# Kernel optimization log

Hardware: AMD Instinct MI355X
Metric: run time of the kernel (lower is better)

## Reference

```python
import jax, jax.numpy as jnp
import numpy as np

B = 262144
IN_DIM, HID, EXP, LAT, N_BLOCKS, N_CODES = 54, 256, 512, 32, 4, 512
EPS = 1e-5


def _layernorm(x, g, b):
    mu = jnp.mean(x, axis=-1, keepdims=True)
    var = jnp.mean(jnp.square(x - mu), axis=-1, keepdims=True)
    return (x - mu) * jax.lax.rsqrt(var + EPS) * g + b


def _blocks(h, ln_g, ln_b, w1, b1, w2, b2):
    # stacked params over n_blocks; small fixed loop over layers
    for i in range(N_BLOCKS):
        y = _layernorm(h, ln_g[i], ln_b[i])
        y = jax.nn.gelu(y @ w1[i] + b1[i], approximate=False)  # torch GELU = erf form
        h = h + (y @ w2[i] + b2[i])
    return h


def setup_inputs() -> dict:
    key = jax.random.key(0)
    ks = jax.random.split(key, 32)
    s = 0.02
    d = {
        "x": jax.random.normal(ks[0], (B, IN_DIM), jnp.float32),
        "enc_proj_w": jax.random.normal(ks[1], (IN_DIM, HID)) * s,
        "enc_proj_b": jnp.zeros((HID,)),
        "enc_ln_g": jnp.ones((N_BLOCKS, HID)),
        "enc_ln_b": jnp.zeros((N_BLOCKS, HID)),
        "enc_w1": jax.random.normal(ks[2], (N_BLOCKS, HID, EXP)) * s,
        "enc_b1": jnp.zeros((N_BLOCKS, EXP)),
        "enc_w2": jax.random.normal(ks[3], (N_BLOCKS, EXP, HID)) * s,
        "enc_b2": jnp.zeros((N_BLOCKS, HID)),
        "enc_norm_g": jnp.ones((HID,)),
        "enc_norm_b": jnp.zeros((HID,)),
        "enc_lat_w": jax.random.normal(ks[4], (HID, LAT)) * s,
        "enc_lat_b": jnp.zeros((LAT,)),
        "codebook": jax.random.normal(ks[5], (N_CODES, LAT)),
        "dec_lat_w": jax.random.normal(ks[6], (LAT, HID)) * s,
        "dec_lat_b": jnp.zeros((HID,)),
        "dec_ln_g": jnp.ones((N_BLOCKS, HID)),
        "dec_ln_b": jnp.zeros((N_BLOCKS, HID)),
        "dec_w1": jax.random.normal(ks[7], (N_BLOCKS, HID, EXP)) * s,
        "dec_b1": jnp.zeros((N_BLOCKS, EXP)),
        "dec_w2": jax.random.normal(ks[8], (N_BLOCKS, EXP, HID)) * s,
        "dec_b2": jnp.zeros((N_BLOCKS, HID)),
        "dec_norm_g": jnp.ones((HID,)),
        "dec_norm_b": jnp.zeros((HID,)),
        "dec_proj_w": jax.random.normal(ks[9], (HID, IN_DIM)) * s,
        "dec_proj_b": jnp.zeros((IN_DIM,)),
    }
    return {k: v.astype(jnp.float32) for k, v in d.items()}


def reference(x, enc_proj_w, enc_proj_b, enc_ln_g, enc_ln_b, enc_w1, enc_b1,
              enc_w2, enc_b2, enc_norm_g, enc_norm_b, enc_lat_w, enc_lat_b,
              codebook, dec_lat_w, dec_lat_b, dec_ln_g, dec_ln_b, dec_w1,
              dec_b1, dec_w2, dec_b2, dec_norm_g, dec_norm_b, dec_proj_w,
              dec_proj_b):
    # encode
    h = x @ enc_proj_w + enc_proj_b
    h = _blocks(h, enc_ln_g, enc_ln_b, enc_w1, enc_b1, enc_w2, enc_b2)
    h = _layernorm(h, enc_norm_g, enc_norm_b)
    z = h @ enc_lat_w + enc_lat_b  # (B, LAT)

    # VQ: nearest code by squared distance (same argmin as cdist)
    d2 = (jnp.sum(z * z, -1, keepdims=True)
          - 2.0 * (z @ codebook.T)
          + jnp.sum(codebook * codebook, -1))  # (B, N_CODES)
    indices = jnp.argmin(d2, axis=-1)
    z_q = codebook[indices]
    commit_loss = jnp.mean(jnp.square(z - jax.lax.stop_gradient(z_q)))
    z_q_st = z + jax.lax.stop_gradient(z_q - z)  # straight-through

    # decode
    h = z_q_st @ dec_lat_w + dec_lat_b
    h = _blocks(h, dec_ln_g, dec_ln_b, dec_w1, dec_b1, dec_w2, dec_b2)
    h = _layernorm(h, dec_norm_g, dec_norm_b)
    x_recon = h @ dec_proj_w + dec_proj_b
    return (x_recon, z_q_st, indices, commit_loss)
```

## Files before the change

kernel.cpp:

```cpp
#include <hip/hip_runtime.h>
#include <math.h>

#define BDIM   262144
#define IN_DIM 54
#define HID    256
#define EXPD   512
#define LAT    32
#define NBLK   4
#define NCODES 512
#define EPS    1e-5

#define BT     512
#define ROWS   32
#define R0S    36

#define O_ZQ   14155776
#define O_IDX  22544384
#define O_LOSS 22806528


template<typename T> __device__ __forceinline__ T gelu_T(T x);
template<> __device__ __forceinline__ double gelu_T<double>(double x) {
    return 0.5 * x * (1.0 + erf(x * 0.70710678118654752440));
}
template<> __device__ __forceinline__ float gelu_T<float>(float x) {
    return 0.5f * x * (1.0f + erff(x * 0.70710678f));
}
template<typename T> __device__ __forceinline__ T rsqrt_T(T x);
template<> __device__ __forceinline__ double rsqrt_T<double>(double x) { return 1.0 / sqrt(x); }
template<> __device__ __forceinline__ float  rsqrt_T<float>(float x)  { return 1.0f / sqrtf(x); }

template<typename T>
__device__ __forceinline__ void ln_to_abuf(T acc[4][4], float* r0,
    const float* __restrict__ g, const float* __restrict__ bta,
    const float* __restrict__ b2, int rt, int ct)
{
    T s[4], sq[4];
    #pragma unroll
    for (int i = 0; i < 4; i++) {
        s[i]  = acc[i][0] + acc[i][1] + acc[i][2] + acc[i][3];
        sq[i] = acc[i][0]*acc[i][0] + acc[i][1]*acc[i][1]
              + acc[i][2]*acc[i][2] + acc[i][3]*acc[i][3];
    }
    #pragma unroll
    for (int m = 1; m < 64; m <<= 1) {
        #pragma unroll
        for (int i = 0; i < 4; i++) {
            s[i]  += __shfl_xor(s[i],  m);
            sq[i] += __shfl_xor(sq[i], m);
        }
    }
    float4 gv = *(const float4*)(g + ct*4);
    float4 bv = *(const float4*)(bta + ct*4);
    float gj[4] = {gv.x, gv.y, gv.z, gv.w};
    float bj[4] = {bv.x, bv.y, bv.z, bv.w};
    T mu[4], rs[4];
    #pragma unroll
    for (int i = 0; i < 4; i++) {
        mu[i] = s[i] * (T)(1.0 / HID);
        T var = sq[i] * (T)(1.0 / HID) - mu[i] * mu[i];
        rs[i] = rsqrt_T<T>(var + (T)EPS);
    }
    #pragma unroll
    for (int j = 0; j < 4; j++) {
        float4 o;
        o.x = (float)((acc[0][j] - mu[0]) * rs[0] * (T)gj[j] + (T)bj[j]);
        o.y = (float)((acc[1][j] - mu[1]) * rs[1] * (T)gj[j] + (T)bj[j]);
        o.z = (float)((acc[2][j] - mu[2]) * rs[2] * (T)gj[j] + (T)bj[j]);
        o.w = (float)((acc[3][j] - mu[3]) * rs[3] * (T)gj[j] + (T)bj[j]);
        *(float4*)(r0 + (ct*4 + j)*R0S + rt*4) = o;
    }
    if (b2) {
        float4 b2v = *(const float4*)(b2 + ct*4);
        float bb[4] = {b2v.x, b2v.y, b2v.z, b2v.w};
        #pragma unroll
        for (int i = 0; i < 4; i++)
            #pragma unroll
            for (int j = 0; j < 4; j++)
                acc[i][j] += (T)bb[j];
    }
}

template<typename T>
__device__ __forceinline__ void ffn_gemm1(T yacc[4][8], const float* __restrict__ W1,
                                          const float* r0, float* r1,
                                          int rt, int ct, int tid)
{
    #pragma unroll
    for (int i = 0; i < 4; i++)
        #pragma unroll
        for (int j = 0; j < 8; j++) yacc[i][j] = 0;
    float4 R[4];
    #pragma unroll
    for (int u = 0; u < 4; u++) R[u] = *(const float4*)(W1 + (tid + BT*u)*4);
    for (int k0 = 0; k0 < HID; k0 += 16) {
        #pragma unroll
        for (int u = 0; u < 4; u++) *(float4*)(r1 + (tid + BT*u)*4) = R[u];
        __syncthreads();
        if (k0 + 16 < HID) {
            const float* src = W1 + (long)(k0 + 16) * EXPD;
            #pragma unroll
            for (int u = 0; u < 4; u++) R[u] = *(const float4*)(src + (tid + BT*u)*4);
        }
        #pragma unroll 2
        for (int k = 0; k < 16; k++) {
            float4 av = *(const float4*)(r0 + (k0 + k)*R0S + rt*4);
            float4 w0 = *(const float4*)(r1 + k*EXPD + ct*4);
            float4 w1 = *(const float4*)(r1 + k*EXPD + 256 + ct*4);
            T a[4]  = {(T)av.x, (T)av.y, (T)av.z, (T)av.w};
            T wv[8] = {(T)w0.x, (T)w0.y, (T)w0.z, (T)w0.w,
                       (T)w1.x, (T)w1.y, (T)w1.z, (T)w1.w};
            #pragma unroll
            for (int i = 0; i < 4; i++)
                #pragma unroll
                for (int j = 0; j < 8; j++)
                    yacc[i][j] += a[i] * wv[j];
        }
        __syncthreads();
    }
}

template<typename T>
__device__ __forceinline__ void gemm2_acc(T acc[4][4], const float* __restrict__ W, int E,
                                          const float* r0, float* r1,
                                          int rt, int ct, int tid)
{
    float4 R[4];
    {
        int n0 = (E < 32 ? E : 32) * 64;
        #pragma unroll
        for (int u = 0; u < 4; u++) {
            int idx = tid + BT*u;
            if (idx < n0) R[u] = *(const float4*)(W + idx*4);
        }
    }
    for (int e0 = 0; e0 < E; e0 += 32) {
        int n = E - e0; if (n > 32) n = 32;
        #pragma unroll
        for (int u = 0; u < 4; u++) {
            int idx = tid + BT*u;
            if (idx < n*64) *(float4*)(r1 + idx*4) = R[u];
        }
        __syncthreads();
        if (e0 + 32 < E) {
            int n2 = E - e0 - 32; if (n2 > 32) n2 = 32;
            const float* src = W + (long)(e0 + 32) * HID;
            #pragma unroll
            for (int u = 0; u < 4; u++) {
                int idx = tid + BT*u;
                if (idx < n2*64) R[u] = *(const float4*)(src + idx*4);
            }
        }
        #pragma unroll 2
        for (int e = 0; e < n; e++) {
            float4 av = *(const float4*)(r0 + (e0 + e)*R0S + rt*4);
            float4 wv = *(const float4*)(r1 + e*HID + ct*4);
            T a[4] = {(T)av.x, (T)av.y, (T)av.z, (T)av.w};
            T w[4] = {(T)wv.x, (T)wv.y, (T)wv.z, (T)wv.w};
            #pragma unroll
            for (int i = 0; i < 4; i++)
                #pragma unroll
                for (int j = 0; j < 4; j++)
                    acc[i][j] += a[i] * w[j];
        }
        __syncthreads();
    }
}

template<typename T>
__device__ __forceinline__ void ffn_layer(T acc[4][4], float* r0, float* r1,
    const float* lng, const float* lnb,
    const float* W1, const float* b1, const float* W2, const float* b2,
    int rt, int ct, int tid)
{
    ln_to_abuf<T>(acc, r0, lng, lnb, b2, rt, ct);
    T yacc[4][8];
    ffn_gemm1<T>(yacc, W1, r0, r1, rt, ct, tid);
    #pragma unroll
    for (int h = 0; h < 2; h++) {
        float4 b1v = *(const float4*)(b1 + h*256 + ct*4);
        float bb[4] = {b1v.x, b1v.y, b1v.z, b1v.w};
        #pragma unroll
        for (int j = 0; j < 4; j++) {
            float4 o;
            o.x = (float)gelu_T<T>(yacc[0][h*4 + j] + (T)bb[j]);
            o.y = (float)gelu_T<T>(yacc[1][h*4 + j] + (T)bb[j]);
            o.z = (float)gelu_T<T>(yacc[2][h*4 + j] + (T)bb[j]);
            o.w = (float)gelu_T<T>(yacc[3][h*4 + j] + (T)bb[j]);
            *(float4*)(r0 + (ct*4 + j)*R0S + rt*4) = o;
        }
        gemm2_acc<T>(acc, W2 + (long)h*256*HID, 256, r0, r1, rt, ct, tid);
    }
}

__global__ __launch_bounds__(BT, 4)
void k_encoder(const float* __restrict__ x,
               const float* __restrict__ epw, const float* __restrict__ epb,
               const float* __restrict__ lng, const float* __restrict__ lnb,
               const float* __restrict__ W1, const float* __restrict__ b1,
               const float* __restrict__ W2, const float* __restrict__ b2,
               const float* __restrict__ ng, const float* __restrict__ nb,
               const float* __restrict__ Wl, const float* __restrict__ bl,
               const float* __restrict__ cb, float* __restrict__ dout)
{
    typedef double T;
    __shared__ __align__(16) char smem[78336];
    float*  r0   = (float*)smem;
    float*  r1   = (float*)(smem + 36864);
    double* zbuf = (double*)(smem + 69632);
    double* ccs  = (double*)(smem + 36864);
    const int tid = threadIdx.x;
    const int rt = tid >> 6, ct = tid & 63;
    const long row0 = (long)blockIdx.x * ROWS;

    #pragma unroll
    for (int u = 0; u < 4; u++) {
        int idx = tid + BT*u;
        if (idx < ROWS * IN_DIM) {
            int r = idx / IN_DIM, c = idx % IN_DIM;
            r0[c*R0S + r] = x[row0*IN_DIM + idx];
        }
    }
    T acc[4][4];
    {
        float4 bv = *(const float4*)(epb + ct*4);
        float bb[4] = {bv.x, bv.y, bv.z, bv.w};
        #pragma unroll
        for (int i = 0; i < 4; i++)
            #pragma unroll
            for (int j = 0; j < 4; j++) acc[i][j] = (T)bb[j];
    }
    gemm2_acc<T>(acc, epw, IN_DIM, r0, r1, rt, ct, tid);

    for (int l = 0; l < NBLK; l++)
        ffn_layer<T>(acc, r0, r1, lng + l*HID, lnb + l*HID,
                     W1 + (long)l*HID*EXPD, b1 + l*EXPD,
                     W2 + (long)l*EXPD*HID, b2 + l*HID, rt, ct, tid);

    ln_to_abuf<T>(acc, r0, ng, nb, nullptr, rt, ct);
    #pragma unroll
    for (int u = 0; u < 4; u++)
        *(float4*)(r1 + (tid + BT*u)*4) = *(const float4*)(Wl + (tid + BT*u)*4);
    __syncthreads();

    const int r = tid >> 4, q = tid & 15;
    {
        float2 blv = *(const float2*)(bl + q*2);
        T z0 = (T)blv.x, z1 = (T)blv.y;
        #pragma unroll 4
        for (int k = 0; k < HID; k++) {
            T a = (T)r0[k*R0S + r];
            float2 w = *(const float2*)(r1 + k*LAT + q*2);
            z0 += a * (T)w.x; z1 += a * (T)w.y;
        }
        zbuf[r*34 + q*2] = z0; zbuf[r*34 + q*2 + 1] = z1;
    }
    __syncthreads();

    {
        const float* cp = cb + (long)tid * LAT;
        T sc = 0;
        #pragma unroll
        for (int j = 0; j < LAT; j += 4) {
            float4 v = *(const float4*)(cp + j);
            sc += (T)v.x*(T)v.x + (T)v.y*(T)v.y + (T)v.z*(T)v.z + (T)v.w*(T)v.w;
        }
        ccs[tid] = sc;
    }
    __syncthreads();

    T bd; int bi;
    {
        T zr[32];
        #pragma unroll
        for (int j = 0; j < LAT; j++) zr[j] = zbuf[r*34 + j];
        T zz = 0;
        #pragma unroll
        for (int j = 0; j < LAT; j++) zz += zr[j]*zr[j];
        bd = (T)1e300; bi = 0;
        for (int c0 = 0; c0 < 32; c0++) {
            int code = q*32 + c0;
            const float* cp = cb + (long)code * LAT;
            T dot = 0;
            #pragma unroll
            for (int j = 0; j < LAT; j += 4) {
                float4 v = *(const float4*)(cp + j);
                dot += zr[j]*(T)v.x + zr[j+1]*(T)v.y + zr[j+2]*(T)v.z + zr[j+3]*(T)v.w;
            }
            T d2 = (zz - 2.0*dot) + ccs[code];
            if (d2 < bd) { bd = d2; bi = code; }
        }
        #pragma unroll
        for (int m = 1; m < 16; m <<= 1) {
            T ob = __shfl_xor(bd, m);
            int obi = __shfl_xor(bi, m);
            if (ob < bd || (ob == bd && obi < bi)) { bd = ob; bi = obi; }
        }
        if (q == 0) {
            long grow = row0 + r;
            dout[O_IDX + grow] = (float)bi;
            const float* cq = cb + (long)bi * LAT;
            #pragma unroll
            for (int j = 0; j < LAT; j += 4)
                *(float4*)(dout + O_ZQ + grow*LAT + j) = *(const float4*)(cq + j);
        }
    }
    __syncthreads();
    T ws = bd;
    ws += __shfl_xor(ws, 16);
    ws += __shfl_xor(ws, 32);
    if ((tid & 63) == 0) zbuf[tid >> 6] = ws;
    __syncthreads();
    if (tid == 0) {
        T t = 0;
        #pragma unroll
        for (int w = 0; w < 8; w++) t += zbuf[w];
        atomicAdd(dout + O_LOSS, (float)t);
    }
}

__global__ __launch_bounds__(BT, 4)
void k_decoder(float* __restrict__ dout,
               const float* __restrict__ Wl, const float* __restrict__ bl,
               const float* __restrict__ lng, const float* __restrict__ lnb,
               const float* __restrict__ W1, const float* __restrict__ b1,
               const float* __restrict__ W2, const float* __restrict__ b2,
               const float* __restrict__ ng, const float* __restrict__ nb,
               const float* __restrict__ Wp, const float* __restrict__ pb)
{
    typedef float T;
    __shared__ __align__(16) char smem[69632];
    float* r0 = (float*)smem;
    float* r1 = (float*)(smem + 36864);
    const int tid = threadIdx.x;
    const int rt = tid >> 6, ct = tid & 63;
    const long row0 = (long)blockIdx.x * ROWS;

    #pragma unroll
    for (int u = 0; u < 2; u++) {
        int idx = tid + BT*u;
        int r = idx >> 5, c = idx & 31;
        r0[c*R0S + r] = dout[O_ZQ + row0*LAT + idx];
    }
    T acc[4][4];
    {
        float4 bv = *(const float4*)(bl + ct*4);
        float bb[4] = {bv.x, bv.y, bv.z, bv.w};
        #pragma unroll
        for (int i = 0; i < 4; i++)
            #pragma unroll
            for (int j = 0; j < 4; j++) acc[i][j] = bb[j];
    }
    gemm2_acc<T>(acc, Wl, LAT, r0, r1, rt, ct, tid);

    for (int l = 0; l < NBLK; l++)
        ffn_layer<T>(acc, r0, r1, lng + l*HID, lnb + l*HID,
                     W1 + (long)l*HID*EXPD, b1 + l*EXPD,
                     W2 + (long)l*EXPD*HID, b2 + l*HID, rt, ct, tid);

    ln_to_abuf<T>(acc, r0, ng, nb, nullptr, rt, ct);

    const int r = tid >> 4, q = tid & 15;
    float oacc[4];
    #pragma unroll
    for (int j = 0; j < 4; j++) {
        int c = q*4 + j;
        oacc[j] = (c < IN_DIM) ? pb[c] : 0.f;
    }
    for (int k0 = 0; k0 < HID; k0 += 128) {
        #pragma unroll
        for (int u = 0; u < 4; u++) {
            int idx = tid + BT*u;
            if (idx < 1728)
                ((float4*)r1)[idx] = ((const float4*)(Wp + (long)k0*IN_DIM))[idx];
        }
        __syncthreads();
        #pragma unroll 4
        for (int k = 0; k < 128; k++) {
            float a = r0[(k0 + k)*R0S + r];
            #pragma unroll
            for (int j = 0; j < 4; j++)
                oacc[j] += a * r1[k*IN_DIM + q*4 + j];
        }
        __syncthreads();
    }
    #pragma unroll
    for (int j = 0; j < 4; j++) {
        int c = q*4 + j;
        if (c < IN_DIM) dout[(row0 + r)*IN_DIM + c] = oacc[j];
    }
}

__global__ void k_zero(float* p) { *p = 0.0f; }
__global__ void k_final(float* p) { *p = *p * (1.0f / 8388608.0f); }

extern "C" void kernel_launch(void* const* d_in, const int* in_sizes, int n_in,
                              void* d_out, int out_size, void* d_ws, size_t ws_size,
                              hipStream_t stream)
{
    (void)in_sizes; (void)n_in; (void)out_size; (void)d_ws; (void)ws_size;
    const float* x     = (const float*)d_in[0];
    const float* epw   = (const float*)d_in[1];
    const float* epb   = (const float*)d_in[2];
    const float* elng  = (const float*)d_in[3];
    const float* elnb  = (const float*)d_in[4];
    const float* ew1   = (const float*)d_in[5];
    const float* eb1   = (const float*)d_in[6];
    const float* ew2   = (const float*)d_in[7];
    const float* eb2   = (const float*)d_in[8];
    const float* eng   = (const float*)d_in[9];
    const float* enb   = (const float*)d_in[10];
    const float* elatw = (const float*)d_in[11];
    const float* elatb = (const float*)d_in[12];
    const float* cbk   = (const float*)d_in[13];
    const float* dlatw = (const float*)d_in[14];
    const float* dlatb = (const float*)d_in[15];
    const float* dlng  = (const float*)d_in[16];
    const float* dlnb  = (const float*)d_in[17];
    const float* dw1   = (const float*)d_in[18];
    const float* db1   = (const float*)d_in[19];
    const float* dw2   = (const float*)d_in[20];
    const float* db2   = (const float*)d_in[21];
    const float* dng   = (const float*)d_in[22];
    const float* dnb   = (const float*)d_in[23];
    const float* dpw   = (const float*)d_in[24];
    const float* dpb   = (const float*)d_in[25];
    float* out = (float*)d_out;

    dim3 blk(BT, 1, 1);
    k_zero<<<1, 1, 0, stream>>>(out + O_LOSS);
    k_encoder<<<BDIM / ROWS, blk, 0, stream>>>(
        x, epw, epb, elng, elnb, ew1, eb1, ew2, eb2, eng, enb, elatw, elatb, cbk, out);
    k_decoder<<<BDIM / ROWS, blk, 0, stream>>>(
        out, dlatw, dlatb, dlng, dlnb, dw1, db1, dw2, db2, dng, dnb, dpw, dpb);
    k_final<<<1, 1, 0, stream>>>(out + O_LOSS);
}
```

Before: 36.18 ms.

## Halve rows per block and remap thread tiles across all encoder/decoder stages

Cuts the rows handled per workgroup from 32 to 16 and reshapes every stage to match. The hidden accumulator becomes 2x4 per thread, the first FFN GEMM uses a 4x4 tile over a 128-column thread map, and the GELU output is written one half at a time. The latent projection, VQ search and output projection are also remapped to the new thread grid. The aim is fewer registers and less LDS per block so more blocks run at once, but each weight tile loaded into LDS is now reused across half as many rows, so weight traffic per row doubles. The launch-bounds occupancy hint also drops from 4 to 2.

```diff
diff --git a/kernel.cpp b/kernel.cpp
--- a/kernel.cpp
+++ b/kernel.cpp
@@ -11,8 +11,8 @@
 #define EPS    1e-5
 
 #define BT     512
-#define ROWS   32
-#define R0S    36
+#define ROWS   16
+#define R0S    20
 
 #define O_ZQ   14155776
 #define O_IDX  22544384
@@ -31,13 +31,13 @@
 template<> __device__ __forceinline__ float  rsqrt_T<float>(float x)  { return 1.0f / sqrtf(x); }
 
 template<typename T>
-__device__ __forceinline__ void ln_to_abuf(T acc[4][4], float* r0,
+__device__ __forceinline__ void ln_to_abuf(T acc[2][4], float* r0,
     const float* __restrict__ g, const float* __restrict__ bta,
     const float* __restrict__ b2, int rt, int ct)
 {
-    T s[4], sq[4];
-    #pragma unroll
-    for (int i = 0; i < 4; i++) {
+    T s[2], sq[2];
+    #pragma unroll
+    for (int i = 0; i < 2; i++) {
         s[i]  = acc[i][0] + acc[i][1] + acc[i][2] + acc[i][3];
         sq[i] = acc[i][0]*acc[i][0] + acc[i][1]*acc[i][1]
               + acc[i][2]*acc[i][2] + acc[i][3]*acc[i][3];
@@ -45,7 +45,7 @@
     #pragma unroll
     for (int m = 1; m < 64; m <<= 1) {
         #pragma unroll
-        for (int i = 0; i < 4; i++) {
+        for (int i = 0; i < 2; i++) {
             s[i]  += __shfl_xor(s[i],  m);
             sq[i] += __shfl_xor(sq[i], m);
         }
@@ -54,27 +54,25 @@
     float4 bv = *(const float4*)(bta + ct*4);
     float gj[4] = {gv.x, gv.y, gv.z, gv.w};
     float bj[4] = {bv.x, bv.y, bv.z, bv.w};
-    T mu[4], rs[4];
-    #pragma unroll
-    for (int i = 0; i < 4; i++) {
+    T mu[2], rs[2];
+    #pragma unroll
+    for (int i = 0; i < 2; i++) {
         mu[i] = s[i] * (T)(1.0 / HID);
         T var = sq[i] * (T)(1.0 / HID) - mu[i] * mu[i];
         rs[i] = rsqrt_T<T>(var + (T)EPS);
     }
     #pragma unroll
     for (int j = 0; j < 4; j++) {
-        float4 o;
+        float2 o;
         o.x = (float)((acc[0][j] - mu[0]) * rs[0] * (T)gj[j] + (T)bj[j]);
         o.y = (float)((acc[1][j] - mu[1]) * rs[1] * (T)gj[j] + (T)bj[j]);
-        o.z = (float)((acc[2][j] - mu[2]) * rs[2] * (T)gj[j] + (T)bj[j]);
-        o.w = (float)((acc[3][j] - mu[3]) * rs[3] * (T)gj[j] + (T)bj[j]);
-        *(float4*)(r0 + (ct*4 + j)*R0S + rt*4) = o;
+        *(float2*)(r0 + (ct*4 + j)*R0S + rt*2) = o;
     }
     if (b2) {
         float4 b2v = *(const float4*)(b2 + ct*4);
         float bb[4] = {b2v.x, b2v.y, b2v.z, b2v.w};
         #pragma unroll
-        for (int i = 0; i < 4; i++)
+        for (int i = 0; i < 2; i++)
             #pragma unroll
             for (int j = 0; j < 4; j++)
                 acc[i][j] += (T)bb[j];
@@ -82,14 +80,14 @@
 }
 
 template<typename T>
-__device__ __forceinline__ void ffn_gemm1(T yacc[4][8], const float* __restrict__ W1,
+__device__ __forceinline__ void ffn_gemm1(T yacc[4][4], const float* __restrict__ W1,
                                           const float* r0, float* r1,
-                                          int rt, int ct, int tid)
+                                          int rt1, int ct1, int tid)
 {
     #pragma unroll
     for (int i = 0; i < 4; i++)
         #pragma unroll
-        for (int j = 0; j < 8; j++) yacc[i][j] = 0;
+        for (int j = 0; j < 4; j++) yacc[i][j] = 0;
     float4 R[4];
     #pragma unroll
     for (int u = 0; u < 4; u++) R[u] = *(const float4*)(W1 + (tid + BT*u)*4);
@@ -104,24 +102,22 @@
         }
         #pragma unroll 2
         for (int k = 0; k < 16; k++) {
-            float4 av = *(const float4*)(r0 + (k0 + k)*R0S + rt*4);
-            float4 w0 = *(const float4*)(r1 + k*EXPD + ct*4);
-            float4 w1 = *(const float4*)(r1 + k*EXPD + 256 + ct*4);
-            T a[4]  = {(T)av.x, (T)av.y, (T)av.z, (T)av.w};
-            T wv[8] = {(T)w0.x, (T)w0.y, (T)w0.z, (T)w0.w,
-                       (T)w1.x, (T)w1.y, (T)w1.z, (T)w1.w};
+            float4 av = *(const float4*)(r0 + (k0 + k)*R0S + rt1*4);
+            float4 wv = *(const float4*)(r1 + k*EXPD + ct1*4);
+            T a[4] = {(T)av.x, (T)av.y, (T)av.z, (T)av.w};
+            T w[4] = {(T)wv.x, (T)wv.y, (T)wv.z, (T)wv.w};
             #pragma unroll
             for (int i = 0; i < 4; i++)
                 #pragma unroll
-                for (int j = 0; j < 8; j++)
-                    yacc[i][j] += a[i] * wv[j];
+                for (int j = 0; j < 4; j++)
+                    yacc[i][j] += a[i] * w[j];
         }
         __syncthreads();
     }
 }
 
 template<typename T>
-__device__ __forceinline__ void gemm2_acc(T acc[4][4], const float* __restrict__ W, int E,
+__device__ __forceinline__ void gemm2_acc(T acc[2][4], const float* __restrict__ W, int E,
                                           const float* r0, float* r1,
                                           int rt, int ct, int tid)
 {
@@ -153,12 +149,12 @@
         }
         #pragma unroll 2
         for (int e = 0; e < n; e++) {
-            float4 av = *(const float4*)(r0 + (e0 + e)*R0S + rt*4);
+            float2 av = *(const float2*)(r0 + (e0 + e)*R0S + rt*2);
             float4 wv = *(const float4*)(r1 + e*HID + ct*4);
-            T a[4] = {(T)av.x, (T)av.y, (T)av.z, (T)av.w};
+            T a[2] = {(T)av.x, (T)av.y};
             T w[4] = {(T)wv.x, (T)wv.y, (T)wv.z, (T)wv.w};
             #pragma unroll
-            for (int i = 0; i < 4; i++)
+            for (int i = 0; i < 2; i++)
                 #pragma unroll
                 for (int j = 0; j < 4; j++)
                     acc[i][j] += a[i] * w[j];
@@ -168,32 +164,35 @@
 }
 
 template<typename T>
-__device__ __forceinline__ void ffn_layer(T acc[4][4], float* r0, float* r1,
+__device__ __forceinline__ void ffn_layer(T acc[2][4], float* r0, float* r1,
     const float* lng, const float* lnb,
     const float* W1, const float* b1, const float* W2, const float* b2,
-    int rt, int ct, int tid)
+    int rt, int ct, int rt1, int ct1, int tid)
 {
     ln_to_abuf<T>(acc, r0, lng, lnb, b2, rt, ct);
-    T yacc[4][8];
-    ffn_gemm1<T>(yacc, W1, r0, r1, rt, ct, tid);
+    T yacc[4][4];
+    ffn_gemm1<T>(yacc, W1, r0, r1, rt1, ct1, tid);
+    const int h1 = ct1 >> 6;
     #pragma unroll
     for (int h = 0; h < 2; h++) {
-        float4 b1v = *(const float4*)(b1 + h*256 + ct*4);
-        float bb[4] = {b1v.x, b1v.y, b1v.z, b1v.w};
-        #pragma unroll
-        for (int j = 0; j < 4; j++) {
-            float4 o;
-            o.x = (float)gelu_T<T>(yacc[0][h*4 + j] + (T)bb[j]);
-            o.y = (float)gelu_T<T>(yacc[1][h*4 + j] + (T)bb[j]);
-            o.z = (float)gelu_T<T>(yacc[2][h*4 + j] + (T)bb[j]);
-            o.w = (float)gelu_T<T>(yacc[3][h*4 + j] + (T)bb[j]);
-            *(float4*)(r0 + (ct*4 + j)*R0S + rt*4) = o;
+        if (h1 == h) {
+            float4 b1v = *(const float4*)(b1 + ct1*4);
+            T bb[4] = {(T)b1v.x, (T)b1v.y, (T)b1v.z, (T)b1v.w};
+            #pragma unroll
+            for (int j = 0; j < 4; j++) {
+                float4 o;
+                o.x = (float)gelu_T<T>(yacc[0][j] + bb[j]);
+                o.y = (float)gelu_T<T>(yacc[1][j] + bb[j]);
+                o.z = (float)gelu_T<T>(yacc[2][j] + bb[j]);
+                o.w = (float)gelu_T<T>(yacc[3][j] + bb[j]);
+                *(float4*)(r0 + ((ct1 & 63)*4 + j)*R0S + rt1*4) = o;
+            }
         }
         gemm2_acc<T>(acc, W2 + (long)h*256*HID, 256, r0, r1, rt, ct, tid);
     }
 }
 
-__global__ __launch_bounds__(BT, 4)
+__global__ __launch_bounds__(BT, 2)
 void k_encoder(const float* __restrict__ x,
                const float* __restrict__ epw, const float* __restrict__ epb,
                const float* __restrict__ lng, const float* __restrict__ lnb,
@@ -204,29 +203,30 @@
                const float* __restrict__ cb, float* __restrict__ dout)
 {
     typedef double T;
-    __shared__ __align__(16) char smem[78336];
+    __shared__ __align__(16) char smem[57600];
     float*  r0   = (float*)smem;
-    float*  r1   = (float*)(smem + 36864);
-    double* zbuf = (double*)(smem + 69632);
-    double* ccs  = (double*)(smem + 36864);
+    float*  r1   = (float*)(smem + 20480);
+    double* zbuf = (double*)(smem + 53248);
+    double* ccs  = (double*)(smem + 20480);
     const int tid = threadIdx.x;
     const int rt = tid >> 6, ct = tid & 63;
+    const int rt1 = tid >> 7, ct1 = tid & 127;
     const long row0 = (long)blockIdx.x * ROWS;
 
     #pragma unroll
-    for (int u = 0; u < 4; u++) {
+    for (int u = 0; u < 2; u++) {
         int idx = tid + BT*u;
         if (idx < ROWS * IN_DIM) {
             int r = idx / IN_DIM, c = idx % IN_DIM;
             r0[c*R0S + r] = x[row0*IN_DIM + idx];
         }
     }
-    T acc[4][4];
+    T acc[2][4];
     {
         float4 bv = *(const float4*)(epb + ct*4);
         float bb[4] = {bv.x, bv.y, bv.z, bv.w};
         #pragma unroll
-        for (int i = 0; i < 4; i++)
+        for (int i = 0; i < 2; i++)
             #pragma unroll
             for (int j = 0; j < 4; j++) acc[i][j] = (T)bb[j];
     }
@@ -235,7 +235,7 @@
     for (int l = 0; l < NBLK; l++)
         ffn_layer<T>(acc, r0, r1, lng + l*HID, lnb + l*HID,
                      W1 + (long)l*HID*EXPD, b1 + l*EXPD,
-                     W2 + (long)l*EXPD*HID, b2 + l*HID, rt, ct, tid);
+                     W2 + (long)l*EXPD*HID, b2 + l*HID, rt, ct, rt1, ct1, tid);
 
     ln_to_abuf<T>(acc, r0, ng, nb, nullptr, rt, ct);
     #pragma unroll
@@ -243,17 +243,15 @@
         *(float4*)(r1 + (tid + BT*u)*4) = *(const float4*)(Wl + (tid + BT*u)*4);
     __syncthreads();
 
-    const int r = tid >> 4, q = tid & 15;
-    {
-        float2 blv = *(const float2*)(bl + q*2);
-        T z0 = (T)blv.x, z1 = (T)blv.y;
+    const int r = tid >> 5, q = tid & 31;
+    {
+        T z = (T)bl[q];
         #pragma unroll 4
         for (int k = 0; k < HID; k++) {
             T a = (T)r0[k*R0S + r];
-            float2 w = *(const float2*)(r1 + k*LAT + q*2);
-            z0 += a * (T)w.x; z1 += a * (T)w.y;
-        }
-        zbuf[r*34 + q*2] = z0; zbuf[r*34 + q*2 + 1] = z1;
+            z += a * (T)r1[k*LAT + q];
+        }
+        zbuf[r*34 + q] = z;
     }
     __syncthreads();
 
@@ -278,8 +276,8 @@
         #pragma unroll
         for (int j = 0; j < LAT; j++) zz += zr[j]*zr[j];
         bd = (T)1e300; bi = 0;
-        for (int c0 = 0; c0 < 32; c0++) {
-            int code = q*32 + c0;
+        for (int c0 = 0; c0 < 16; c0++) {
+            int code = q*16 + c0;
             const float* cp = cb + (long)code * LAT;
             T dot = 0;
             #pragma unroll
@@ -291,7 +289,7 @@
             if (d2 < bd) { bd = d2; bi = code; }
         }
         #pragma unroll
-        for (int m = 1; m < 16; m <<= 1) {
+        for (int m = 1; m < 32; m <<= 1) {
             T ob = __shfl_xor(bd, m);
             int obi = __shfl_xor(bi, m);
             if (ob < bd || (ob == bd && obi < bi)) { bd = ob; bi = obi; }
@@ -307,7 +305,6 @@
     }
     __syncthreads();
     T ws = bd;
-    ws += __shfl_xor(ws, 16);
     ws += __shfl_xor(ws, 32);
     if ((tid & 63) == 0) zbuf[tid >> 6] = ws;
     __syncthreads();
@@ -319,7 +316,7 @@
     }
 }
 
-__global__ __launch_bounds__(BT, 4)
+__global__ __launch_bounds__(BT, 2)
 void k_decoder(float* __restrict__ dout,
                const float* __restrict__ Wl, const float* __restrict__ bl,
                const float* __restrict__ lng, const float* __restrict__ lnb,
@@ -329,25 +326,25 @@
                const float* __restrict__ Wp, const float* __restrict__ pb)
 {
     typedef float T;
-    __shared__ __align__(16) char smem[69632];
+    __shared__ __align__(16) char smem[53248];
     float* r0 = (float*)smem;
-    float* r1 = (float*)(smem + 36864);
+    float* r1 = (float*)(smem + 20480);
     const int tid = threadIdx.x;
     const int rt = tid >> 6, ct = tid & 63;
+    const int rt1 = tid >> 7, ct1 = tid & 127;
     const long row0 = (long)blockIdx.x * ROWS;
 
-    #pragma unroll
-    for (int u = 0; u < 2; u++) {
-        int idx = tid + BT*u;
+    {
+        int idx = tid;
         int r = idx >> 5, c = idx & 31;
         r0[c*R0S + r] = dout[O_ZQ + row0*LAT + idx];
     }
-    T acc[4][4];
+    T acc[2][4];
     {
         float4 bv = *(const float4*)(bl + ct*4);
         float bb[4] = {bv.x, bv.y, bv.z, bv.w};
         #pragma unroll
-        for (int i = 0; i < 4; i++)
+        for (int i = 0; i < 2; i++)
             #pragma unroll
             for (int j = 0; j < 4; j++) acc[i][j] = bb[j];
     }
@@ -356,15 +353,15 @@
     for (int l = 0; l < NBLK; l++)
         ffn_layer<T>(acc, r0, r1, lng + l*HID, lnb + l*HID,
                      W1 + (long)l*HID*EXPD, b1 + l*EXPD,
-                     W2 + (long)l*EXPD*HID, b2 + l*HID, rt, ct, tid);
+                     W2 + (long)l*EXPD*HID, b2 + l*HID, rt, ct, rt1, ct1, tid);
 
     ln_to_abuf<T>(acc, r0, ng, nb, nullptr, rt, ct);
 
-    const int r = tid >> 4, q = tid & 15;
-    float oacc[4];
-    #pragma unroll
-    for (int j = 0; j < 4; j++) {
-        int c = q*4 + j;
+    const int r = tid >> 5, q = tid & 31;
+    float oacc[2];
+    #pragma unroll
+    for (int j = 0; j < 2; j++) {
+        int c = q*2 + j;
         oacc[j] = (c < IN_DIM) ? pb[c] : 0.f;
     }
     for (int k0 = 0; k0 < HID; k0 += 128) {
@@ -379,14 +376,14 @@
         for (int k = 0; k < 128; k++) {
             float a = r0[(k0 + k)*R0S + r];
             #pragma unroll
-            for (int j = 0; j < 4; j++)
-                oacc[j] += a * r1[k*IN_DIM + q*4 + j];
-        }
-        __syncthreads();
-    }
-    #pragma unroll
-    for (int j = 0; j < 4; j++) {
-        int c = q*4 + j;
+            for (int j = 0; j < 2; j++)
+                oacc[j] += a * r1[k*IN_DIM + q*2 + j];
+        }
+        __syncthreads();
+    }
+    #pragma unroll
+    for (int j = 0; j < 2; j++) {
+        int c = q*2 + j;
         if (c < IN_DIM) dout[(row0 + r)*IN_DIM + c] = oacc[j];
     }
 }
```

Measured after the change: 61.33 ms. 1.7x slower.

## Run encoder with 1024-thread blocks and smaller per-thread double tiles

Applied to the files above, without the earlier changes.

The encoder, which accumulates in fp64, now launches 1024 threads per block instead of 512. Each thread holds a 2x4 residual tile and a 4x4 GEMM1 tile, with 32/64-deep shared-memory weight stages and a 32-lane VQ argmin. The goal is to lower fp64 register pressure and raise the number of active waves, so the expensive double FMAs hide latency better. The trade-offs are more shared memory per block (about 108 KB), more redundant shared loads per FLOP, and fewer codes scanned per thread. The decoder is split into its own float-only helpers and its launch bound changes to (512, 2).

```diff
diff --git a/kernel.cpp b/kernel.cpp
--- a/kernel.cpp
+++ b/kernel.cpp
@@ -10,34 +10,31 @@
 #define NCODES 512
 #define EPS    1e-5
 
-#define BT     512
 #define ROWS   32
 #define R0S    36
+#define BTE    1024
+#define BTD    512
 
 #define O_ZQ   14155776
 #define O_IDX  22544384
 #define O_LOSS 22806528
 
 
-template<typename T> __device__ __forceinline__ T gelu_T(T x);
-template<> __device__ __forceinline__ double gelu_T<double>(double x) {
+__device__ __forceinline__ double gelu_d(double x) {
     return 0.5 * x * (1.0 + erf(x * 0.70710678118654752440));
 }
-template<> __device__ __forceinline__ float gelu_T<float>(float x) {
+__device__ __forceinline__ float gelu_f(float x) {
     return 0.5f * x * (1.0f + erff(x * 0.70710678f));
 }
-template<typename T> __device__ __forceinline__ T rsqrt_T(T x);
-template<> __device__ __forceinline__ double rsqrt_T<double>(double x) { return 1.0 / sqrt(x); }
-template<> __device__ __forceinline__ float  rsqrt_T<float>(float x)  { return 1.0f / sqrtf(x); }
-
-template<typename T>
-__device__ __forceinline__ void ln_to_abuf(T acc[4][4], float* r0,
+
+
+__device__ __forceinline__ void ln_e(double acc[2][4], float* r0,
     const float* __restrict__ g, const float* __restrict__ bta,
     const float* __restrict__ b2, int rt, int ct)
 {
-    T s[4], sq[4];
-    #pragma unroll
-    for (int i = 0; i < 4; i++) {
+    double s[2], sq[2];
+    #pragma unroll
+    for (int i = 0; i < 2; i++) {
         s[i]  = acc[i][0] + acc[i][1] + acc[i][2] + acc[i][3];
         sq[i] = acc[i][0]*acc[i][0] + acc[i][1]*acc[i][1]
               + acc[i][2]*acc[i][2] + acc[i][3]*acc[i][3];
@@ -45,7 +42,7 @@
     #pragma unroll
     for (int m = 1; m < 64; m <<= 1) {
         #pragma unroll
-        for (int i = 0; i < 4; i++) {
+        for (int i = 0; i < 2; i++) {
             s[i]  += __shfl_xor(s[i],  m);
             sq[i] += __shfl_xor(sq[i], m);
         }
@@ -54,146 +51,140 @@
     float4 bv = *(const float4*)(bta + ct*4);
     float gj[4] = {gv.x, gv.y, gv.z, gv.w};
     float bj[4] = {bv.x, bv.y, bv.z, bv.w};
-    T mu[4], rs[4];
-    #pragma unroll
-    for (int i = 0; i < 4; i++) {
-        mu[i] = s[i] * (T)(1.0 / HID);
-        T var = sq[i] * (T)(1.0 / HID) - mu[i] * mu[i];
-        rs[i] = rsqrt_T<T>(var + (T)EPS);
+    double mu[2], rs[2];
+    #pragma unroll
+    for (int i = 0; i < 2; i++) {
+        mu[i] = s[i] * (1.0 / HID);
+        double var = sq[i] * (1.0 / HID) - mu[i] * mu[i];
+        rs[i] = 1.0 / sqrt(var + EPS);
     }
     #pragma unroll
     for (int j = 0; j < 4; j++) {
-        float4 o;
-        o.x = (float)((acc[0][j] - mu[0]) * rs[0] * (T)gj[j] + (T)bj[j]);
-        o.y = (float)((acc[1][j] - mu[1]) * rs[1] * (T)gj[j] + (T)bj[j]);
-        o.z = (float)((acc[2][j] - mu[2]) * rs[2] * (T)gj[j] + (T)bj[j]);
-        o.w = (float)((acc[3][j] - mu[3]) * rs[3] * (T)gj[j] + (T)bj[j]);
-        *(float4*)(r0 + (ct*4 + j)*R0S + rt*4) = o;
+        float2 o;
+        o.x = (float)((acc[0][j] - mu[0]) * rs[0] * (double)gj[j] + (double)bj[j]);
+        o.y = (float)((acc[1][j] - mu[1]) * rs[1] * (double)gj[j] + (double)bj[j]);
+        *(float2*)(r0 + (ct*4 + j)*R0S + rt*2) = o;
     }
     if (b2) {
         float4 b2v = *(const float4*)(b2 + ct*4);
         float bb[4] = {b2v.x, b2v.y, b2v.z, b2v.w};
         #pragma unroll
-        for (int i = 0; i < 4; i++)
+        for (int i = 0; i < 2; i++)
             #pragma unroll
             for (int j = 0; j < 4; j++)
-                acc[i][j] += (T)bb[j];
-    }
-}
-
-template<typename T>
-__device__ __forceinline__ void ffn_gemm1(T yacc[4][8], const float* __restrict__ W1,
-                                          const float* r0, float* r1,
-                                          int rt, int ct, int tid)
+                acc[i][j] += (double)bb[j];
+    }
+}
+
+__device__ __forceinline__ void gemm1_e(double yacc[4][4], const float* __restrict__ W1,
+                                        const float* r0, float* r1, int rt1, int ct1, int tid)
 {
     #pragma unroll
     for (int i = 0; i < 4; i++)
         #pragma unroll
-        for (int j = 0; j < 8; j++) yacc[i][j] = 0;
+        for (int j = 0; j < 4; j++) yacc[i][j] = 0;
     float4 R[4];
     #pragma unroll
-    for (int u = 0; u < 4; u++) R[u] = *(const float4*)(W1 + (tid + BT*u)*4);
-    for (int k0 = 0; k0 < HID; k0 += 16) {
-        #pragma unroll
-        for (int u = 0; u < 4; u++) *(float4*)(r1 + (tid + BT*u)*4) = R[u];
-        __syncthreads();
-        if (k0 + 16 < HID) {
-            const float* src = W1 + (long)(k0 + 16) * EXPD;
-            #pragma unroll
-            for (int u = 0; u < 4; u++) R[u] = *(const float4*)(src + (tid + BT*u)*4);
+    for (int u = 0; u < 4; u++) R[u] = *(const float4*)(W1 + (tid + BTE*u)*4);
+    for (int k0 = 0; k0 < HID; k0 += 32) {
+        #pragma unroll
+        for (int u = 0; u < 4; u++) *(float4*)(r1 + (tid + BTE*u)*4) = R[u];
+        __syncthreads();
+        if (k0 + 32 < HID) {
+            const float* src = W1 + (long)(k0 + 32) * EXPD;
+            #pragma unroll
+            for (int u = 0; u < 4; u++) R[u] = *(const float4*)(src + (tid + BTE*u)*4);
         }
         #pragma unroll 2
-        for (int k = 0; k < 16; k++) {
-            float4 av = *(const float4*)(r0 + (k0 + k)*R0S + rt*4);
-            float4 w0 = *(const float4*)(r1 + k*EXPD + ct*4);
-            float4 w1 = *(const float4*)(r1 + k*EXPD + 256 + ct*4);
-            T a[4]  = {(T)av.x, (T)av.y, (T)av.z, (T)av.w};
-            T wv[8] = {(T)w0.x, (T)w0.y, (T)w0.z, (T)w0.w,
-                       (T)w1.x, (T)w1.y, (T)w1.z, (T)w1.w};
-            #pragma unroll
-            for (int i = 0; i < 4; i++)
-                #pragma unroll
-                for (int j = 0; j < 8; j++)
-                    yacc[i][j] += a[i] * wv[j];
-        }
-        __syncthreads();
-    }
-}
-
-template<typename T>
-__device__ __forceinline__ void gemm2_acc(T acc[4][4], const float* __restrict__ W, int E,
-                                          const float* r0, float* r1,
-                                          int rt, int ct, int tid)
-{
-    float4 R[4];
-    {
-        int n0 = (E < 32 ? E : 32) * 64;
-        #pragma unroll
-        for (int u = 0; u < 4; u++) {
-            int idx = tid + BT*u;
-            if (idx < n0) R[u] = *(const float4*)(W + idx*4);
-        }
-    }
-    for (int e0 = 0; e0 < E; e0 += 32) {
-        int n = E - e0; if (n > 32) n = 32;
-        #pragma unroll
-        for (int u = 0; u < 4; u++) {
-            int idx = tid + BT*u;
-            if (idx < n*64) *(float4*)(r1 + idx*4) = R[u];
-        }
-        __syncthreads();
-        if (e0 + 32 < E) {
-            int n2 = E - e0 - 32; if (n2 > 32) n2 = 32;
-            const float* src = W + (long)(e0 + 32) * HID;
-            #pragma unroll
-            for (int u = 0; u < 4; u++) {
-                int idx = tid + BT*u;
-                if (idx < n2*64) R[u] = *(const float4*)(src + idx*4);
-            }
-        }
-        #pragma unroll 2
-        for (int e = 0; e < n; e++) {
-            float4 av = *(const float4*)(r0 + (e0 + e)*R0S + rt*4);
-            float4 wv = *(const float4*)(r1 + e*HID + ct*4);
-            T a[4] = {(T)av.x, (T)av.y, (T)av.z, (T)av.w};
-            T w[4] = {(T)wv.x, (T)wv.y, (T)wv.z, (T)wv.w};
+        for (int k = 0; k < 32; k++) {
+            float4 av = *(const float4*)(r0 + (k0 + k)*R0S + rt1*4);
+            float4 wv = *(const float4*)(r1 + k*EXPD + ct1*4);
+            double a[4] = {(double)av.x, (double)av.y, (double)av.z, (double)av.w};
+            double w[4] = {(double)wv.x, (double)wv.y, (double)wv.z, (double)wv.w};
             #pragma unroll
             for (int i = 0; i < 4; i++)
                 #pragma unroll
                 for (int j = 0; j < 4; j++)
+                    yacc[i][j] += a[i] * w[j];
+        }
+        __syncthreads();
+    }
+}
+
+__device__ __forceinline__ void gemm2_e(double acc[2][4], const float* __restrict__ W, int E,
+                                        const float* r0, float* r1, int rt, int ct, int tid)
+{
+    float4 R[4];
+    {
+        int n0 = (E < 64 ? E : 64) * 64;
+        #pragma unroll
+        for (int u = 0; u < 4; u++) {
+            int idx = tid + BTE*u;
+            if (idx < n0) R[u] = *(const float4*)(W + idx*4);
+        }
+    }
+    for (int e0 = 0; e0 < E; e0 += 64) {
+        int n = E - e0; if (n > 64) n = 64;
+        #pragma unroll
+        for (int u = 0; u < 4; u++) {
+            int idx = tid + BTE*u;
+            if (idx < n*64) *(float4*)(r1 + idx*4) = R[u];
+        }
+        __syncthreads();
+        if (e0 + 64 < E) {
+            int n2 = E - e0 - 64; if (n2 > 64) n2 = 64;
+            const float* src = W + (long)(e0 + 64) * HID;
+            #pragma unroll
+            for (int u = 0; u < 4; u++) {
+                int idx = tid + BTE*u;
+                if (idx < n2*64) R[u] = *(const float4*)(src + idx*4);
+            }
+        }
+        #pragma unroll 2
+        for (int e = 0; e < n; e++) {
+            float2 av = *(const float2*)(r0 + (e0 + e)*R0S + rt*2);
+            float4 wv = *(const float4*)(r1 + e*HID + ct*4);
+            double a[2] = {(double)av.x, (double)av.y};
+            double w[4] = {(double)wv.x, (double)wv.y, (double)wv.z, (double)wv.w};
+            #pragma unroll
+            for (int i = 0; i < 2; i++)
+                #pragma unroll
+                for (int j = 0; j < 4; j++)
                     acc[i][j] += a[i] * w[j];
         }
         __syncthreads();
     }
 }
 
-template<typename T>
-__device__ __forceinline__ void ffn_layer(T acc[4][4], float* r0, float* r1,
+__device__ __forceinline__ void ffn_layer_e(double acc[2][4], float* r0, float* r1,
     const float* lng, const float* lnb,
     const float* W1, const float* b1, const float* W2, const float* b2,
-    int rt, int ct, int tid)
-{
-    ln_to_abuf<T>(acc, r0, lng, lnb, b2, rt, ct);
-    T yacc[4][8];
-    ffn_gemm1<T>(yacc, W1, r0, r1, rt, ct, tid);
+    int rt, int ct, int rt1, int ct1, int tid)
+{
+    ln_e(acc, r0, lng, lnb, b2, rt, ct);
+    double yacc[4][4];
+    gemm1_e(yacc, W1, r0, r1, rt1, ct1, tid);
+    const int h1 = ct1 >> 6;
     #pragma unroll
     for (int h = 0; h < 2; h++) {
-        float4 b1v = *(const float4*)(b1 + h*256 + ct*4);
-        float bb[4] = {b1v.x, b1v.y, b1v.z, b1v.w};
-        #pragma unroll
-        for (int j = 0; j < 4; j++) {
-            float4 o;
-            o.x = (float)gelu_T<T>(yacc[0][h*4 + j] + (T)bb[j]);
-            o.y = (float)gelu_T<T>(yacc[1][h*4 + j] + (T)bb[j]);
-            o.z = (float)gelu_T<T>(yacc[2][h*4 + j] + (T)bb[j]);
-            o.w = (float)gelu_T<T>(yacc[3][h*4 + j] + (T)bb[j]);
-            *(float4*)(r0 + (ct*4 + j)*R0S + rt*4) = o;
-        }
-        gemm2_acc<T>(acc, W2 + (long)h*256*HID, 256, r0, r1, rt, ct, tid);
-    }
-}
-
-__global__ __launch_bounds__(BT, 4)
+        if (h1 == h) {
+            float4 b1v = *(const float4*)(b1 + ct1*4);
+            double bb[4] = {(double)b1v.x, (double)b1v.y, (double)b1v.z, (double)b1v.w};
+            #pragma unroll
+            for (int j = 0; j < 4; j++) {
+                float4 o;
+                o.x = (float)gelu_d(yacc[0][j] + bb[j]);
+                o.y = (float)gelu_d(yacc[1][j] + bb[j]);
+                o.z = (float)gelu_d(yacc[2][j] + bb[j]);
+                o.w = (float)gelu_d(yacc[3][j] + bb[j]);
+                *(float4*)(r0 + ((ct1 & 63)*4 + j)*R0S + rt1*4) = o;
+            }
+        }
+        gemm2_e(acc, W2 + (long)h*256*HID, 256, r0, r1, rt, ct, tid);
+    }
+}
+
+__global__ __launch_bounds__(BTE)
 void k_encoder(const float* __restrict__ x,
                const float* __restrict__ epw, const float* __restrict__ epb,
                const float* __restrict__ lng, const float* __restrict__ lnb,
@@ -203,96 +194,96 @@
                const float* __restrict__ Wl, const float* __restrict__ bl,
                const float* __restrict__ cb, float* __restrict__ dout)
 {
-    typedef double T;
-    __shared__ __align__(16) char smem[78336];
+    __shared__ __align__(16) char smem[111104];
     float*  r0   = (float*)smem;
     float*  r1   = (float*)(smem + 36864);
-    double* zbuf = (double*)(smem + 69632);
+    double* zbuf = (double*)(smem + 102400);
     double* ccs  = (double*)(smem + 36864);
     const int tid = threadIdx.x;
     const int rt = tid >> 6, ct = tid & 63;
+    const int rt1 = tid >> 7, ct1 = tid & 127;
     const long row0 = (long)blockIdx.x * ROWS;
 
     #pragma unroll
-    for (int u = 0; u < 4; u++) {
-        int idx = tid + BT*u;
+    for (int u = 0; u < 2; u++) {
+        int idx = tid + BTE*u;
         if (idx < ROWS * IN_DIM) {
             int r = idx / IN_DIM, c = idx % IN_DIM;
             r0[c*R0S + r] = x[row0*IN_DIM + idx];
         }
     }
-    T acc[4][4];
+    double acc[2][4];
     {
         float4 bv = *(const float4*)(epb + ct*4);
         float bb[4] = {bv.x, bv.y, bv.z, bv.w};
         #pragma unroll
-        for (int i = 0; i < 4; i++)
-            #pragma unroll
-            for (int j = 0; j < 4; j++) acc[i][j] = (T)bb[j];
-    }
-    gemm2_acc<T>(acc, epw, IN_DIM, r0, r1, rt, ct, tid);
+        for (int i = 0; i < 2; i++)
+            #pragma unroll
+            for (int j = 0; j < 4; j++) acc[i][j] = (double)bb[j];
+    }
+    gemm2_e(acc, epw, IN_DIM, r0, r1, rt, ct, tid);
 
     for (int l = 0; l < NBLK; l++)
-        ffn_layer<T>(acc, r0, r1, lng + l*HID, lnb + l*HID,
-                     W1 + (long)l*HID*EXPD, b1 + l*EXPD,
-                     W2 + (long)l*EXPD*HID, b2 + l*HID, rt, ct, tid);
-
-    ln_to_abuf<T>(acc, r0, ng, nb, nullptr, rt, ct);
-    #pragma unroll
-    for (int u = 0; u < 4; u++)
-        *(float4*)(r1 + (tid + BT*u)*4) = *(const float4*)(Wl + (tid + BT*u)*4);
+        ffn_layer_e(acc, r0, r1, lng + l*HID, lnb + l*HID,
+                    W1 + (long)l*HID*EXPD, b1 + l*EXPD,
+                    W2 + (long)l*EXPD*HID, b2 + l*HID, rt, ct, rt1, ct1, tid);
+
+    ln_e(acc, r0, ng, nb, nullptr, rt, ct);
+    #pragma unroll
+    for (int u = 0; u < 2; u++)
+        *(float4*)(r1 + (tid + BTE*u)*4) = *(const float4*)(Wl + (tid + BTE*u)*4);
     __syncthreads();
 
-    const int r = tid >> 4, q = tid & 15;
+    const int r = tid >> 5, q = tid & 31;
     {
-        float2 blv = *(const float2*)(bl + q*2);
-        T z0 = (T)blv.x, z1 = (T)blv.y;
+        double z = (double)bl[q];
         #pragma unroll 4
         for (int k = 0; k < HID; k++) {
-            T a = (T)r0[k*R0S + r];
-            float2 w = *(const float2*)(r1 + k*LAT + q*2);
-            z0 += a * (T)w.x; z1 += a * (T)w.y;
-        }
-        zbuf[r*34 + q*2] = z0; zbuf[r*34 + q*2 + 1] = z1;
+            double a = (double)r0[k*R0S + r];
+            z += a * (double)r1[k*LAT + q];
+        }
+        zbuf[r*34 + q] = z;
     }
     __syncthreads();
 
-    {
+    if (tid < NCODES) {
         const float* cp = cb + (long)tid * LAT;
-        T sc = 0;
+        double sc = 0;
         #pragma unroll
         for (int j = 0; j < LAT; j += 4) {
             float4 v = *(const float4*)(cp + j);
-            sc += (T)v.x*(T)v.x + (T)v.y*(T)v.y + (T)v.z*(T)v.z + (T)v.w*(T)v.w;
+            sc += (double)v.x*(double)v.x + (double)v.y*(double)v.y
+                + (double)v.z*(double)v.z + (double)v.w*(double)v.w;
         }
         ccs[tid] = sc;
     }
     __syncthreads();
 
-    T bd; int bi;
+    double bd; int bi;
     {
-        T zr[32];
+        double zr[32];
         #pragma unroll
         for (int j = 0; j < LAT; j++) zr[j] = zbuf[r*34 + j];
-        T zz = 0;
+        double zz = 0;
         #pragma unroll
         for (int j = 0; j < LAT; j++) zz += zr[j]*zr[j];
-        bd = (T)1e300; bi = 0;
-        for (int c0 = 0; c0 < 32; c0++) {
-            int code = q*32 + c0;
+        bd = 1e300; bi = 0;
+        for (int c0 = 0; c0 < 16; c0++) {
+            int code = q*16 + c0;
             const float* cp = cb + (long)code * LAT;
-            T dot = 0;
+            double dot = 0;
             #pragma unroll
             for (int j = 0; j < LAT; j += 4) {
                 float4 v = *(const float4*)(cp + j);
-                dot += zr[j]*(T)v.x + zr[j+1]*(T)v.y + zr[j+2]*(T)v.z + zr[j+3]*(T)v.w;
+                dot += zr[j]*(double)v.x + zr[j+1]*(double)v.y
+                     + zr[j+2]*(double)v.z + zr[j+3]*(double)v.w;
             }
-            T d2 = (zz - 2.0*dot) + ccs[code];
+            double d2 = (zz - 2.0*dot) + ccs[code];
             if (d2 < bd) { bd = d2; bi = code; }
         }
         #pragma unroll
-        for (int m = 1; m < 16; m <<= 1) {
-            T ob = __shfl_xor(bd, m);
+        for (int m = 1; m < 32; m <<= 1) {
+            double ob = __shfl_xor(bd, m);
             int obi = __shfl_xor(bi, m);
             if (ob < bd || (ob == bd && obi < bi)) { bd = ob; bi = obi; }
         }
@@ -306,20 +297,176 @@
         }
     }
     __syncthreads();
-    T ws = bd;
-    ws += __shfl_xor(ws, 16);
+    double ws = bd;
     ws += __shfl_xor(ws, 32);
     if ((tid & 63) == 0) zbuf[tid >> 6] = ws;
     __syncthreads();
     if (tid == 0) {
-        T t = 0;
-        #pragma unroll
-        for (int w = 0; w < 8; w++) t += zbuf[w];
+        double t = 0;
+        #pragma unroll
+        for (int w = 0; w < 16; w++) t += zbuf[w];
         atomicAdd(dout + O_LOSS, (float)t);
     }
 }
 
-__global__ __launch_bounds__(BT, 4)
+
+__device__ __forceinline__ void ln_d(float acc[4][4], float* r0,
+    const float* __restrict__ g, const float* __restrict__ bta,
+    const float* __restrict__ b2, int rt, int ct)
+{
+    float s[4], sq[4];
+    #pragma unroll
+    for (int i = 0; i < 4; i++) {
+        s[i]  = acc[i][0] + acc[i][1] + acc[i][2] + acc[i][3];
+        sq[i] = acc[i][0]*acc[i][0] + acc[i][1]*acc[i][1]
+              + acc[i][2]*acc[i][2] + acc[i][3]*acc[i][3];
+    }
+    #pragma unroll
+    for (int m = 1; m < 64; m <<= 1) {
+        #pragma unroll
+        for (int i = 0; i < 4; i++) {
+            s[i]  += __shfl_xor(s[i],  m);
+            sq[i] += __shfl_xor(sq[i], m);
+        }
+    }
+    float4 gv = *(const float4*)(g + ct*4);
+    float4 bv = *(const float4*)(bta + ct*4);
+    float gj[4] = {gv.x, gv.y, gv.z, gv.w};
+    float bj[4] = {bv.x, bv.y, bv.z, bv.w};
+    float mu[4], rs[4];
+    #pragma unroll
+    for (int i = 0; i < 4; i++) {
+        mu[i] = s[i] * (1.0f / HID);
+        float var = sq[i] * (1.0f / HID) - mu[i] * mu[i];
+        rs[i] = 1.0f / sqrtf(var + (float)EPS);
+    }
+    #pragma unroll
+    for (int j = 0; j < 4; j++) {
+        float4 o;
+        o.x = (acc[0][j] - mu[0]) * rs[0] * gj[j] + bj[j];
+        o.y = (acc[1][j] - mu[1]) * rs[1] * gj[j] + bj[j];
+        o.z = (acc[2][j] - mu[2]) * rs[2] * gj[j] + bj[j];
+        o.w = (acc[3][j] - mu[3]) * rs[3] * gj[j] + bj[j];
+        *(float4*)(r0 + (ct*4 + j)*R0S + rt*4) = o;
+    }
+    if (b2) {
+        float4 b2v = *(const float4*)(b2 + ct*4);
+        float bb[4] = {b2v.x, b2v.y, b2v.z, b2v.w};
+        #pragma unroll
+        for (int i = 0; i < 4; i++)
+            #pragma unroll
+            for (int j = 0; j < 4; j++)
+                acc[i][j] += bb[j];
+    }
+}
+
+__device__ __forceinline__ void gemm1_d(float yacc[4][8], const float* __restrict__ W1,
+                                        const float* r0, float* r1, int rt, int ct, int tid)
+{
+    #pragma unroll
+    for (int i = 0; i < 4; i++)
+        #pragma unroll
+        for (int j = 0; j < 8; j++) yacc[i][j] = 0;
+    float4 R[4];
+    #pragma unroll
+    for (int u = 0; u < 4; u++) R[u] = *(const float4*)(W1 + (tid + BTD*u)*4);
+    for (int k0 = 0; k0 < HID; k0 += 16) {
+        #pragma unroll
+        for (int u = 0; u < 4; u++) *(float4*)(r1 + (tid + BTD*u)*4) = R[u];
+        __syncthreads();
+        if (k0 + 16 < HID) {
+            const float* src = W1 + (long)(k0 + 16) * EXPD;
+            #pragma unroll
+            for (int u = 0; u < 4; u++) R[u] = *(const float4*)(src + (tid + BTD*u)*4);
+        }
+        #pragma unroll 2
+        for (int k = 0; k < 16; k++) {
+            float4 av = *(const float4*)(r0 + (k0 + k)*R0S + rt*4);
+            float4 w0 = *(const float4*)(r1 + k*EXPD + ct*4);
+            float4 w1 = *(const float4*)(r1 + k*EXPD + 256 + ct*4);
+            float a[4]  = {av.x, av.y, av.z, av.w};
+            float wv[8] = {w0.x, w0.y, w0.z, w0.w, w1.x, w1.y, w1.z, w1.w};
+            #pragma unroll
+            for (int i = 0; i < 4; i++)
+                #pragma unroll
+                for (int j = 0; j < 8; j++)
+                    yacc[i][j] += a[i] * wv[j];
+        }
+        __syncthreads();
+    }
+}
+
+__device__ __forceinline__ void gemm2_d(float acc[4][4], const float* __restrict__ W, int E,
+                                        const float* r0, float* r1, int rt, int ct, int tid)
+{
+    float4 R[4];
+    {
+        int n0 = (E < 32 ? E : 32) * 64;
+        #pragma unroll
+        for (int u = 0; u < 4; u++) {
+            int idx = tid + BTD*u;
+            if (idx < n0) R[u] = *(const float4*)(W + idx*4);
+        }
+    }
+    for (int e0 = 0; e0 < E; e0 += 32) {
+        int n = E - e0; if (n > 32) n = 32;
+        #pragma unroll
+        for (int u = 0; u < 4; u++) {
+            int idx = tid + BTD*u;
+            if (idx < n*64) *(float4*)(r1 + idx*4) = R[u];
+        }
+        __syncthreads();
+        if (e0 + 32 < E) {
+            int n2 = E - e0 - 32; if (n2 > 32) n2 = 32;
+            const float* src = W + (long)(e0 + 32) * HID;
+            #pragma unroll
+            for (int u = 0; u < 4; u++) {
+                int idx = tid + BTD*u;
+                if (idx < n2*64) R[u] = *(const float4*)(src + idx*4);
+            }
+        }
+        #pragma unroll 2
+        for (int e = 0; e < n; e++) {
+            float4 av = *(const float4*)(r0 + (e0 + e)*R0S + rt*4);
+            float4 wv = *(const float4*)(r1 + e*HID + ct*4);
+            float a[4] = {av.x, av.y, av.z, av.w};
+            float w[4] = {wv.x, wv.y, wv.z, wv.w};
+            #pragma unroll
+            for (int i = 0; i < 4; i++)
+                #pragma unroll
+                for (int j = 0; j < 4; j++)
+                    acc[i][j] += a[i] * w[j];
+        }
+        __syncthreads();
+    }
+}
+
+__device__ __forceinline__ void ffn_layer_d(float acc[4][4], float* r0, float* r1,
+    const float* lng, const float* lnb,
+    const float* W1, const float* b1, const float* W2, const float* b2,
+    int rt, int ct, int tid)
+{
+    ln_d(acc, r0, lng, lnb, b2, rt, ct);
+    float yacc[4][8];
+    gemm1_d(yacc, W1, r0, r1, rt, ct, tid);
+    #pragma unroll
+    for (int h = 0; h < 2; h++) {
+        float4 b1v = *(const float4*)(b1 + h*256 + ct*4);
+        float bb[4] = {b1v.x, b1v.y, b1v.z, b1v.w};
+        #pragma unroll
+        for (int j = 0; j < 4; j++) {
+            float4 o;
+            o.x = gelu_f(yacc[0][h*4 + j] + bb[j]);
+            o.y = gelu_f(yacc[1][h*4 + j] + bb[j]);
+            o.z = gelu_f(yacc[2][h*4 + j] + bb[j]);
+            o.w = gelu_f(yacc[3][h*4 + j] + bb[j]);
+            *(float4*)(r0 + (ct*4 + j)*R0S + rt*4) = o;
+        }
+        gemm2_d(acc, W2 + (long)h*256*HID, 256, r0, r1, rt, ct, tid);
+    }
+}
+
+__global__ __launch_bounds__(BTD, 2)
 void k_decoder(float* __restrict__ dout,
                const float* __restrict__ Wl, const float* __restrict__ bl,
                const float* __restrict__ lng, const float* __restrict__ lnb,
@@ -328,7 +475,6 @@
                const float* __restrict__ ng, const float* __restrict__ nb,
                const float* __restrict__ Wp, const float* __restrict__ pb)
 {
-    typedef float T;
     __shared__ __align__(16) char smem[69632];
     float* r0 = (float*)smem;
     float* r1 = (float*)(smem + 36864);
@@ -338,11 +484,11 @@
 
     #pragma unroll
     for (int u = 0; u < 2; u++) {
-        int idx = tid + BT*u;
+        int idx = tid + BTD*u;
         int r = idx >> 5, c = idx & 31;
         r0[c*R0S + r] = dout[O_ZQ + row0*LAT + idx];
     }
-    T acc[4][4];
+    float acc[4][4];
     {
         float4 bv = *(const float4*)(bl + ct*4);
         float bb[4] = {bv.x, bv.y, bv.z, bv.w};
@@ -351,14 +497,14 @@
             #pragma unroll
             for (int j = 0; j < 4; j++) acc[i][j] = bb[j];
     }
-    gemm2_acc<T>(acc, Wl, LAT, r0, r1, rt, ct, tid);
+    gemm2_d(acc, Wl, LAT, r0, r1, rt, ct, tid);
 
     for (int l = 0; l < NBLK; l++)
-        ffn_layer<T>(acc, r0, r1, lng + l*HID, lnb + l*HID,
-                     W1 + (long)l*HID*EXPD, b1 + l*EXPD,
-                     W2 + (long)l*EXPD*HID, b2 + l*HID, rt, ct, tid);
-
-    ln_to_abuf<T>(acc, r0, ng, nb, nullptr, rt, ct);
+        ffn_layer_d(acc, r0, r1, lng + l*HID, lnb + l*HID,
+                    W1 + (long)l*HID*EXPD, b1 + l*EXPD,
+                    W2 + (long)l*EXPD*HID, b2 + l*HID, rt, ct, tid);
+
+    ln_d(acc, r0, ng, nb, nullptr, rt, ct);
 
     const int r = tid >> 4, q = tid & 15;
     float oacc[4];
@@ -370,7 +516,7 @@
     for (int k0 = 0; k0 < HID; k0 += 128) {
         #pragma unroll
         for (int u = 0; u < 4; u++) {
-            int idx = tid + BT*u;
+            int idx = tid + BTD*u;
             if (idx < 1728)
                 ((float4*)r1)[idx] = ((const float4*)(Wp + (long)k0*IN_DIM))[idx];
         }
@@ -427,11 +573,10 @@
     const float* dpb   = (const float*)d_in[25];
     float* out = (float*)d_out;
 
-    dim3 blk(BT, 1, 1);
     k_zero<<<1, 1, 0, stream>>>(out + O_LOSS);
-    k_encoder<<<BDIM / ROWS, blk, 0, stream>>>(
+    k_encoder<<<BDIM / ROWS, dim3(BTE), 0, stream>>>(
         x, epw, epb, elng, elnb, ew1, eb1, ew2, eb2, eng, enb, elatw, elatb, cbk, out);
-    k_decoder<<<BDIM / ROWS, blk, 0, stream>>>(
+    k_decoder<<<BDIM / ROWS, dim3(BTD), 0, stream>>>(
         out, dlatw, dlatb, dlng, dlnb, dw1, db1, dw2, db2, dng, dnb, dpw, dpb);
     k_final<<<1, 1, 0, stream>>>(out + O_LOSS);
 }
```

New measurement: 43.13 ms. +19.2%, slower.
